# Kernel tuning notes

Hardware: AMD Instinct MI355X
Metric: run time of the kernel (lower is better)

The kernel has to match this reference:

```python
import jax, jax.numpy as jnp
import numpy as np

B, NPG, NFEAT, NHID, NCLASS = 32, 256, 128, 64, 6
N = B * NPG
E_PER = NPG * 16
C = 1.0
SQC = 1.0  # sqrt(c)
MIN_NORM = 1e-15
PROJ_EPS = 4e-3
LAMB = 1.0


def _norm(x):
    return jnp.clip(jnp.linalg.norm(x, axis=-1, keepdims=True), MIN_NORM)


def artanh(x):
    x = jnp.clip(x, -1.0 + 1e-7, 1.0 - 1e-7)
    return 0.5 * (jnp.log1p(x) - jnp.log1p(-x))


def proj(x):
    # clip points to stay inside the Poincare ball
    n = _norm(x)
    maxn = (1.0 - PROJ_EPS) / SQC
    return jnp.where(n > maxn, x / n * maxn, x)


def expmap0(u):
    un = _norm(u)
    return jnp.tanh(SQC * un) * u / (SQC * un)


def logmap0(p):
    pn = _norm(p)
    return artanh(SQC * pn) * p / (SQC * pn)


def mobius_matvec(W, x):
    xn = _norm(x)
    mx = x @ W.T
    mxn = _norm(mx)
    return jnp.tanh(mxn / xn * artanh(SQC * xn)) * mx / (mxn * SQC)


def mobius_add(x, y):
    x2 = jnp.sum(x * x, -1, keepdims=True)
    y2 = jnp.sum(y * y, -1, keepdims=True)
    xy = jnp.sum(x * y, -1, keepdims=True)
    num = (1.0 + 2.0 * C * xy + C * y2) * x + (1.0 - C * x2) * y
    den = 1.0 + 2.0 * C * xy + C * C * x2 * y2
    return num / jnp.clip(den, MIN_NORM)


def hgc_layer(xh, adj, W, b):
    # HypLinear (mobius matvec + hyperbolic bias)
    h = proj(mobius_matvec(W, xh))
    hb = proj(expmap0(b.reshape(1, -1)))
    h = proj(mobius_add(h, hb))
    # HypAgg: aggregate in tangent space at origin
    h = proj(expmap0(adj @ logmap0(h)))
    # HypAct: relu in tangent space
    return proj(expmap0(jax.nn.relu(logmap0(h))))


def hgpsl_pool(x, adj, att, nb, npg):
    deg = adj.sum(-1)
    dis = jnp.where(deg > 0, deg ** -0.5, 0.0)
    prop = dis[:, None] * (adj @ (dis[:, None] * x))
    score = jnp.abs(x - prop).sum(-1)  # [N]
    k = npg // 2
    vals, idx = jax.lax.top_k(score.reshape(nb, npg), k)  # per-graph top-k
    gidx = (idx + (jnp.arange(nb) * npg)[:, None]).reshape(-1)  # global ids
    xn = x[gidx] * jnp.tanh(vals).reshape(-1, 1)
    adj_ind = adj[gidx][:, gidx]
    # structure learning: single-head additive attention, masked per graph
    d = xn.shape[-1]
    e = jax.nn.leaky_relu((xn @ att[:d])[:, None] + (xn @ att[d:])[None, :], 0.2)
    gid = jnp.repeat(jnp.arange(nb), k)
    mask = gid[:, None] == gid[None, :]
    new_adj = jnp.where(mask, jax.nn.relu(e) + LAMB * adj_ind, 0.0)
    return xn, new_adj


def readout(x, nb, k):
    xr = x.reshape(nb, k, -1)
    return jnp.concatenate([xr.max(axis=1), xr.mean(axis=1)], axis=-1)


def to_hyp(t):
    return proj(expmap0(t))  # proj_tan0 is identity on the Poincare ball


def forward(x, edge_index, W1, b1, W2, b2, W3, b3, att1, att2,
            lw1, lb1, lw2, lb2, lw3, lb3):
    row, col = edge_index[0], edge_index[1]
    w = (x[row].sum(-1) + x[col].sum(-1)) * 0.5
    adj1 = jnp.zeros((N, N), x.dtype).at[row, col].set(w)

    t = logmap0(hgc_layer(to_hyp(x), adj1, W1, b1))
    t, adj2 = hgpsl_pool(t, adj1, att1, B, NPG)
    k1 = NPG // 2
    x1 = readout(t, B, k1)

    t = logmap0(hgc_layer(to_hyp(t), adj2, W2, b2))
    t, adj3 = hgpsl_pool(t, adj2, att2, B, k1)
    k2 = k1 // 2
    x2 = readout(t, B, k2)

    t = logmap0(hgc_layer(to_hyp(t), adj3, W3, b3))
    x3 = readout(t, B, k2)

    r = jax.nn.relu(x1) + jax.nn.relu(x2) + jax.nn.relu(x3)
    r = jax.nn.relu(r @ lw1.T + lb1)
    r = jax.nn.relu(r @ lw2.T + lb2)
    return jax.nn.log_softmax(r @ lw3.T + lb3, axis=-1)


def setup_inputs() -> dict:
    key = jax.random.key(0)
    ks = jax.random.split(key, 16)
    s = 0.1
    x = jax.random.normal(ks[0], (N, NFEAT), jnp.float32)
    off = jnp.repeat(jnp.arange(B, dtype=jnp.int32) * NPG, E_PER)
    row = jax.random.randint(ks[1], (B * E_PER,), 0, NPG, jnp.int32) + off
    col = jax.random.randint(ks[2], (B * E_PER,), 0, NPG, jnp.int32) + off
    edge_index = jnp.stack([row, col])
    return {
        "x": x,
        "edge_index": edge_index,
        "W1": jax.random.normal(ks[3], (NHID, NFEAT), jnp.float32) * s,
        "b1": jax.random.normal(ks[4], (NHID,), jnp.float32) * s,
        "W2": jax.random.normal(ks[5], (NHID, NHID), jnp.float32) * s,
        "b2": jax.random.normal(ks[6], (NHID,), jnp.float32) * s,
        "W3": jax.random.normal(ks[7], (NHID, NHID), jnp.float32) * s,
        "b3": jax.random.normal(ks[8], (NHID,), jnp.float32) * s,
        "att1": jax.random.normal(ks[9], (2 * NHID,), jnp.float32) * s,
        "att2": jax.random.normal(ks[10], (2 * NHID,), jnp.float32) * s,
        "lw1": jax.random.normal(ks[11], (NHID, 2 * NHID), jnp.float32) * s,
        "lb1": jnp.zeros((NHID,), jnp.float32),
        "lw2": jax.random.normal(ks[12], (NHID // 2, NHID), jnp.float32) * s,
        "lb2": jnp.zeros((NHID // 2,), jnp.float32),
        "lw3": jax.random.normal(ks[13], (NCLASS, NHID // 2), jnp.float32) * s,
        "lb3": jnp.zeros((NCLASS,), jnp.float32),
    }


def reference(x, edge_index, W1, b1, W2, b2, W3, b3, att1, att2,
              lw1, lb1, lw2, lb2, lw3, lb3):
    return forward(x, edge_index, W1, b1, W2, b2, W3, b3, att1, att2,
                   lw1, lb1, lw2, lb2, lw3, lb3)
```

## Files before the change

kernel.cpp:

```cpp
#include <hip/hip_runtime.h>
#include <math.h>

#define MAXN 0.996f

__device__ __forceinline__ float wredsum(float v) {
#pragma unroll
  for (int o = 32; o > 0; o >>= 1) v += __shfl_xor(v, o);
  return v;
}

__device__ __forceinline__ float artanh_f(float x) {
  x = fminf(fmaxf(x, -1.0f + 1e-7f), 1.0f - 1e-7f);
  return 0.5f * (log1pf(x) - log1pf(-x));
}

__global__ void k_rowsum(const float* __restrict__ x, float* __restrict__ s) {
  const int row = blockIdx.x, j = threadIdx.x;
  float a = x[(size_t)row * 128 + j] + x[(size_t)row * 128 + 64 + j];
  a = wredsum(a);
  if (j == 0) s[row] = a;
}

__global__ void k_edges(const int* __restrict__ er, const int* __restrict__ ec,
                        const float* __restrict__ s, float* __restrict__ adj, int nE) {
  int e = blockIdx.x * blockDim.x + threadIdx.x;
  if (e >= nE) return;
  int r = er[e], c = ec[e];
  int g = r >> 8;
  adj[(((size_t)g * 256) + (r & 255)) * 256 + (c & 255)] = 0.5f * (s[r] + s[c]);
}

template <int IND>
__global__ void k_stageA(const float* __restrict__ x, const float* __restrict__ Wm,
                         const float* __restrict__ b, float* __restrict__ u) {
  const int row = blockIdx.x;
  const int j = threadIdx.x;
  __shared__ float xs[IND];
  for (int t = j; t < IND; t += 64) xs[t] = x[(size_t)row * IND + t];
  __syncthreads();

  float bj = b[j];
  float nb = sqrtf(wredsum(bj * bj));
  float ub = fmaxf(nb, 1e-15f);
  float eb = tanhf(ub) / ub;
  float cb = fmaxf(eb * nb, 1e-15f);
  float hbj = bj * eb * ((cb > MAXN) ? MAXN / cb : 1.0f);
  float y2 = wredsum(hbj * hbj);

  float a2 = 0.f;
  for (int t = j; t < IND; t += 64) a2 += xs[t] * xs[t];
  float nx = sqrtf(wredsum(a2));
  float un = fmaxf(nx, 1e-15f);
  float s1 = tanhf(un) / un;
  float nv = s1 * nx;
  float nn = fmaxf(nv, 1e-15f);
  float s2 = (nn > MAXN) ? MAXN / nn : 1.0f;
  float alpha = s1 * s2;
  float xn = fmaxf(fminf(nn, MAXN), 1e-15f);

  float y = 0.f;
  const float* wr = Wm + (size_t)j * IND;
  for (int t = 0; t < IND; ++t) y += xs[t] * wr[t];
  float mxj = alpha * y;
  float mxn = fmaxf(sqrtf(wredsum(mxj * mxj)), 1e-15f);
  float hj = (tanhf(mxn / xn * artanh_f(xn)) / mxn) * mxj;

  float hn = fmaxf(sqrtf(wredsum(hj * hj)), 1e-15f);
  if (hn > MAXN) hj *= MAXN / hn;

  float x2 = wredsum(hj * hj);
  float xy = wredsum(hj * hbj);
  float num = (1.f + 2.f * xy + y2) * hj + (1.f - x2) * hbj;
  float den = fmaxf(1.f + 2.f * xy + x2 * y2, 1e-15f);
  float aj = num / den;

  float an = fmaxf(sqrtf(wredsum(aj * aj)), 1e-15f);
  float pn = an;
  if (an > MAXN) { aj *= MAXN / an; pn = MAXN; }
  u[(size_t)row * 64 + j] = (artanh_f(pn) / pn) * aj;
}

template <int NPGL>
__global__ void k_stageB(const float* __restrict__ adj, const float* __restrict__ u,
                         float* __restrict__ t, float* __restrict__ dis, int wantDis) {
  const int row = blockIdx.x;
  const int g = row / NPGL;
  const int j = threadIdx.x;
  const float* arow = adj + (size_t)row * NPGL;
  const float* ug = u + (size_t)g * NPGL * 64;
  float acc = 0.f, dsum = 0.f;
  for (int c = 0; c < NPGL; ++c) { float a = arow[c]; acc += a * ug[(size_t)c * 64 + j]; dsum += a; }

  float n0 = sqrtf(wredsum(acc * acc));
  float u0 = fmaxf(n0, 1e-15f);
  float e1 = tanhf(u0) / u0;
  float c1 = fmaxf(e1 * n0, 1e-15f);
  float v = acc * e1;
  if (c1 > MAXN) { v *= MAXN / c1; c1 = MAXN; }
  v *= artanh_f(c1) / c1;
  v = fmaxf(v, 0.f);

  float n2 = sqrtf(wredsum(v * v));
  float u2 = fmaxf(n2, 1e-15f);
  float e2 = tanhf(u2) / u2;
  float c2 = fmaxf(e2 * n2, 1e-15f);
  v *= e2;
  if (c2 > MAXN) { v *= MAXN / c2; c2 = MAXN; }
  v *= artanh_f(c2) / c2;
  t[(size_t)row * 64 + j] = v;
  if (wantDis && j == 0) dis[row] = (dsum > 0.f) ? (1.0f / sqrtf(dsum)) : 0.f;
}

template <int NPGL>
__global__ void k_stageC(const float* __restrict__ adj, const float* __restrict__ t,
                         const float* __restrict__ dis, float* __restrict__ score) {
  const int row = blockIdx.x;
  const int g = row / NPGL;
  const int j = threadIdx.x;
  const float* arow = adj + (size_t)row * NPGL;
  const float* tg = t + (size_t)g * NPGL * 64;
  const float* dg = dis + (size_t)g * NPGL;
  float acc = 0.f;
  for (int c = 0; c < NPGL; ++c) acc += arow[c] * dg[c] * tg[(size_t)c * 64 + j];
  float d = fabsf(t[(size_t)row * 64 + j] - dis[row] * acc);
  d = wredsum(d);
  if (j == 0) score[row] = d;
}

template <int NPGL>
__global__ void k_stageD(const float* __restrict__ score, const float* __restrict__ t,
                         const float* __restrict__ att, float* __restrict__ xn,
                         float* __restrict__ s1o, float* __restrict__ s2o,
                         int* __restrict__ gidx, float* __restrict__ xread) {
  constexpr int K = NPGL / 2;
  const int g = blockIdx.x;
  const int i = threadIdx.x;
  __shared__ float sc[NPGL];
  __shared__ int sel[K];
  __shared__ float sval[K];
  __shared__ float xs[K * 64];
  sc[i] = score[(size_t)g * NPGL + i];
  __syncthreads();
  float si = sc[i];
  int rank = 0;
  for (int c = 0; c < NPGL; ++c) { float v = sc[c]; rank += (v > si) || (v == si && c < i); }
  if (rank < K) { sel[rank] = i; sval[rank] = si; }
  __syncthreads();
  if (i < K) {
    int li = sel[i];
    float tv = tanhf(sval[i]);
    const float* trow = t + ((size_t)g * NPGL + li) * 64;
    float a = 0.f, b = 0.f;
    for (int jj = 0; jj < 64; ++jj) {
      float v = trow[jj] * tv;
      xs[i * 64 + jj] = v;
      a += v * att[jj];
      b += v * att[64 + jj];
    }
    s1o[(size_t)g * K + i] = a;
    s2o[(size_t)g * K + i] = b;
    gidx[(size_t)g * K + i] = li;
    float* xout = xn + ((size_t)g * K + i) * 64;
    for (int jj = 0; jj < 64; ++jj) xout[jj] = xs[i * 64 + jj];
  }
  __syncthreads();
  if (i < 64) {
    float mx = -1e30f, sm = 0.f;
    for (int r = 0; r < K; ++r) { float v = xs[r * 64 + i]; mx = fmaxf(mx, v); sm += v; }
    xread[(size_t)g * 128 + i] = mx;
    xread[(size_t)g * 128 + 64 + i] = sm * (1.0f / K);
  }
}

template <int NPGL>
__global__ void k_stageE(const float* __restrict__ s1, const float* __restrict__ s2,
                         const int* __restrict__ gidx, const float* __restrict__ adj_old,
                         float* __restrict__ adj_new) {
  constexpr int K = NPGL / 2;
  int idx = blockIdx.x * blockDim.x + threadIdx.x;
  if (idx >= 32 * K * K) return;
  int g = idx / (K * K);
  int r = idx - g * K * K;
  int ii = r / K, jj = r - ii * K;
  float e = s1[(size_t)g * K + ii] + s2[(size_t)g * K + jj];
  float v = fmaxf(e, 0.f) +
            adj_old[(((size_t)g * NPGL) + gidx[(size_t)g * K + ii]) * NPGL + gidx[(size_t)g * K + jj]];
  adj_new[(((size_t)g * K) + ii) * K + jj] = v;
}

__global__ void k_readout64(const float* __restrict__ t, float* __restrict__ xread) {
  const int g = blockIdx.x, j = threadIdx.x;
  float mx = -1e30f, sm = 0.f;
  for (int r = 0; r < 64; ++r) { float v = t[((size_t)g * 64 + r) * 64 + j]; mx = fmaxf(mx, v); sm += v; }
  xread[(size_t)g * 128 + j] = mx;
  xread[(size_t)g * 128 + 64 + j] = sm * (1.0f / 64.0f);
}

__global__ void k_mlp(const float* __restrict__ x1, const float* __restrict__ x2,
                      const float* __restrict__ x3, const float* __restrict__ lw1,
                      const float* __restrict__ lb1, const float* __restrict__ lw2,
                      const float* __restrict__ lb2, const float* __restrict__ lw3,
                      const float* __restrict__ lb3, float* __restrict__ out) {
  const int b = blockIdx.x, j = threadIdx.x;
  __shared__ float r[128];
  __shared__ float h1[64];
  __shared__ float h2[32];
  __shared__ float z[6];
  for (int t = j; t < 128; t += 64)
    r[t] = fmaxf(x1[(size_t)b * 128 + t], 0.f) + fmaxf(x2[(size_t)b * 128 + t], 0.f) +
           fmaxf(x3[(size_t)b * 128 + t], 0.f);
  __syncthreads();
  float acc = lb1[j];
  for (int t = 0; t < 128; ++t) acc += r[t] * lw1[(size_t)j * 128 + t];
  h1[j] = fmaxf(acc, 0.f);
  __syncthreads();
  if (j < 32) {
    float a = lb2[j];
    for (int t = 0; t < 64; ++t) a += h1[t] * lw2[(size_t)j * 64 + t];
    h2[j] = fmaxf(a, 0.f);
  }
  __syncthreads();
  if (j < 6) {
    float a = lb3[j];
    for (int t = 0; t < 32; ++t) a += h2[t] * lw3[(size_t)j * 32 + t];
    z[j] = a;
  }
  __syncthreads();
  if (j < 6) {
    float m = z[0];
    for (int c = 1; c < 6; ++c) m = fmaxf(m, z[c]);
    float se = 0.f;
    for (int c = 0; c < 6; ++c) se += expf(z[c] - m);
    out[(size_t)b * 6 + j] = z[j] - m - logf(se);
  }
}

extern "C" void kernel_launch(void* const* d_in, const int* in_sizes, int n_in,
                              void* d_out, int out_size, void* d_ws, size_t ws_size,
                              hipStream_t stream) {
  const float* x = (const float*)d_in[0];
  const int* ei = (const int*)d_in[1];
  const float* W1 = (const float*)d_in[2];
  const float* b1 = (const float*)d_in[3];
  const float* W2 = (const float*)d_in[4];
  const float* b2 = (const float*)d_in[5];
  const float* W3 = (const float*)d_in[6];
  const float* b3 = (const float*)d_in[7];
  const float* att1 = (const float*)d_in[8];
  const float* att2 = (const float*)d_in[9];
  const float* lw1 = (const float*)d_in[10];
  const float* lb1 = (const float*)d_in[11];
  const float* lw2 = (const float*)d_in[12];
  const float* lb2 = (const float*)d_in[13];
  const float* lw3 = (const float*)d_in[14];
  const float* lb3 = (const float*)d_in[15];
  float* out = (float*)d_out;
  const int nE = in_sizes[1] / 2;

  float* p = (float*)d_ws;
  float* srow = p;  p += 8192;
  float* adj1 = p;  p += (size_t)32 * 256 * 256;
  float* adj2 = p;  p += (size_t)32 * 128 * 128;
  float* adj3 = p;  p += (size_t)32 * 64 * 64;
  float* ubuf = p;  p += (size_t)8192 * 64;
  float* t1 = p;    p += (size_t)8192 * 64;
  float* t2 = p;    p += (size_t)4096 * 64;
  float* t3 = p;    p += (size_t)2048 * 64;
  float* dis = p;   p += 8192;
  float* score = p; p += 8192;
  float* xn1 = p;   p += (size_t)4096 * 64;
  float* xn2 = p;   p += (size_t)2048 * 64;
  float* s1b = p;   p += 4096;
  float* s2b = p;   p += 4096;
  float* x1 = p;    p += 32 * 128;
  float* x2 = p;    p += 32 * 128;
  float* x3 = p;    p += 32 * 128;
  int* gidx1 = (int*)p; p += 4096;
  int* gidx2 = (int*)p; p += 2048;

  hipMemsetAsync(adj1, 0, (size_t)32 * 256 * 256 * sizeof(float), stream);
  k_rowsum<<<8192, 64, 0, stream>>>(x, srow);
  k_edges<<<(nE + 255) / 256, 256, 0, stream>>>(ei, ei + nE, srow, adj1, nE);

  k_stageA<128><<<8192, 64, 0, stream>>>(x, W1, b1, ubuf);
  k_stageB<256><<<8192, 64, 0, stream>>>(adj1, ubuf, t1, dis, 1);
  k_stageC<256><<<8192, 64, 0, stream>>>(adj1, t1, dis, score);
  k_stageD<256><<<32, 256, 0, stream>>>(score, t1, att1, xn1, s1b, s2b, gidx1, x1);
  k_stageE<256><<<(32 * 128 * 128 + 255) / 256, 256, 0, stream>>>(s1b, s2b, gidx1, adj1, adj2);

  k_stageA<64><<<4096, 64, 0, stream>>>(xn1, W2, b2, ubuf);
  k_stageB<128><<<4096, 64, 0, stream>>>(adj2, ubuf, t2, dis, 1);
  k_stageC<128><<<4096, 64, 0, stream>>>(adj2, t2, dis, score);
  k_stageD<128><<<32, 128, 0, stream>>>(score, t2, att2, xn2, s1b, s2b, gidx2, x2);
  k_stageE<128><<<(32 * 64 * 64 + 255) / 256, 256, 0, stream>>>(s1b, s2b, gidx2, adj2, adj3);

  k_stageA<64><<<2048, 64, 0, stream>>>(xn2, W3, b3, ubuf);
  k_stageB<64><<<2048, 64, 0, stream>>>(adj3, ubuf, t3, dis, 0);
  k_readout64<<<32, 64, 0, stream>>>(t3, x3);

  k_mlp<<<32, 64, 0, stream>>>(x1, x2, x3, lw1, lb1, lw2, lb2, lw3, lb3, out);
}
```

Measured before the change: 257.4 us.

## Fuse whole pipeline into per-graph megakernel with sparse CSR aggregation

Replaces the chain of about 15 launches with two kernels: a batched first HypLinear stage that also computes row sums, and a per-graph 1024-thread megakernel. The megakernel builds the adjacency, compresses each row into a per-row neighbour list via ballot, runs sparse aggregation and scoring, and does top-k, pooling, the later layers and the MLP head in one block. This removes launch overhead and the dense 256-wide adjacency scans, at the cost of only 32 blocks of parallelism and a 128-entry cap on neighbours per row. It also assumes edges come sorted by graph with an equal count per graph (EPG = nE/32), which the old scatter did not require.

Result: slower. 763.6 us (+196.7%).

```diff
diff --git a/kernel.cpp b/kernel.cpp
--- a/kernel.cpp
+++ b/kernel.cpp
@@ -2,6 +2,18 @@
 #include <math.h>
 
 #define MAXN 0.996f
+#define AR (1 << 18)
+#define O_ADJ1 0
+#define O_ADJ2 65536
+#define O_ADJ3 81920
+#define O_U 86016
+#define O_T 102400
+#define O_DT 118784
+#define O_XN 135168
+#define O_XN2 143360
+#define O_NZW 147456
+#define O_NZC 180224
+#define O_SROW 212992
 
 __device__ __forceinline__ float wredsum(float v) {
 #pragma unroll
@@ -14,83 +26,7 @@
   return 0.5f * (log1pf(x) - log1pf(-x));
 }
 
-__global__ void k_rowsum(const float* __restrict__ x, float* __restrict__ s) {
-  const int row = blockIdx.x, j = threadIdx.x;
-  float a = x[(size_t)row * 128 + j] + x[(size_t)row * 128 + 64 + j];
-  a = wredsum(a);
-  if (j == 0) s[row] = a;
-}
-
-__global__ void k_edges(const int* __restrict__ er, const int* __restrict__ ec,
-                        const float* __restrict__ s, float* __restrict__ adj, int nE) {
-  int e = blockIdx.x * blockDim.x + threadIdx.x;
-  if (e >= nE) return;
-  int r = er[e], c = ec[e];
-  int g = r >> 8;
-  adj[(((size_t)g * 256) + (r & 255)) * 256 + (c & 255)] = 0.5f * (s[r] + s[c]);
-}
-
-template <int IND>
-__global__ void k_stageA(const float* __restrict__ x, const float* __restrict__ Wm,
-                         const float* __restrict__ b, float* __restrict__ u) {
-  const int row = blockIdx.x;
-  const int j = threadIdx.x;
-  __shared__ float xs[IND];
-  for (int t = j; t < IND; t += 64) xs[t] = x[(size_t)row * IND + t];
-  __syncthreads();
-
-  float bj = b[j];
-  float nb = sqrtf(wredsum(bj * bj));
-  float ub = fmaxf(nb, 1e-15f);
-  float eb = tanhf(ub) / ub;
-  float cb = fmaxf(eb * nb, 1e-15f);
-  float hbj = bj * eb * ((cb > MAXN) ? MAXN / cb : 1.0f);
-  float y2 = wredsum(hbj * hbj);
-
-  float a2 = 0.f;
-  for (int t = j; t < IND; t += 64) a2 += xs[t] * xs[t];
-  float nx = sqrtf(wredsum(a2));
-  float un = fmaxf(nx, 1e-15f);
-  float s1 = tanhf(un) / un;
-  float nv = s1 * nx;
-  float nn = fmaxf(nv, 1e-15f);
-  float s2 = (nn > MAXN) ? MAXN / nn : 1.0f;
-  float alpha = s1 * s2;
-  float xn = fmaxf(fminf(nn, MAXN), 1e-15f);
-
-  float y = 0.f;
-  const float* wr = Wm + (size_t)j * IND;
-  for (int t = 0; t < IND; ++t) y += xs[t] * wr[t];
-  float mxj = alpha * y;
-  float mxn = fmaxf(sqrtf(wredsum(mxj * mxj)), 1e-15f);
-  float hj = (tanhf(mxn / xn * artanh_f(xn)) / mxn) * mxj;
-
-  float hn = fmaxf(sqrtf(wredsum(hj * hj)), 1e-15f);
-  if (hn > MAXN) hj *= MAXN / hn;
-
-  float x2 = wredsum(hj * hj);
-  float xy = wredsum(hj * hbj);
-  float num = (1.f + 2.f * xy + y2) * hj + (1.f - x2) * hbj;
-  float den = fmaxf(1.f + 2.f * xy + x2 * y2, 1e-15f);
-  float aj = num / den;
-
-  float an = fmaxf(sqrtf(wredsum(aj * aj)), 1e-15f);
-  float pn = an;
-  if (an > MAXN) { aj *= MAXN / an; pn = MAXN; }
-  u[(size_t)row * 64 + j] = (artanh_f(pn) / pn) * aj;
-}
-
-template <int NPGL>
-__global__ void k_stageB(const float* __restrict__ adj, const float* __restrict__ u,
-                         float* __restrict__ t, float* __restrict__ dis, int wantDis) {
-  const int row = blockIdx.x;
-  const int g = row / NPGL;
-  const int j = threadIdx.x;
-  const float* arow = adj + (size_t)row * NPGL;
-  const float* ug = u + (size_t)g * NPGL * 64;
-  float acc = 0.f, dsum = 0.f;
-  for (int c = 0; c < NPGL; ++c) { float a = arow[c]; acc += a * ug[(size_t)c * 64 + j]; dsum += a; }
-
+__device__ __forceinline__ float bchain(float acc) {
   float n0 = sqrtf(wredsum(acc * acc));
   float u0 = fmaxf(n0, 1e-15f);
   float e1 = tanhf(u0) / u0;
@@ -99,7 +35,6 @@
   if (c1 > MAXN) { v *= MAXN / c1; c1 = MAXN; }
   v *= artanh_f(c1) / c1;
   v = fmaxf(v, 0.f);
-
   float n2 = sqrtf(wredsum(v * v));
   float u2 = fmaxf(n2, 1e-15f);
   float e2 = tanhf(u2) / u2;
@@ -107,131 +42,341 @@
   v *= e2;
   if (c2 > MAXN) { v *= MAXN / c2; c2 = MAXN; }
   v *= artanh_f(c2) / c2;
-  t[(size_t)row * 64 + j] = v;
-  if (wantDis && j == 0) dis[row] = (dsum > 0.f) ? (1.0f / sqrtf(dsum)) : 0.f;
+  return v;
+}
+
+__global__ __launch_bounds__(256) void k_A1srow(const float* __restrict__ x,
+                                                const float* __restrict__ W1,
+                                                const float* __restrict__ b1,
+                                                float* __restrict__ ws) {
+  constexpr int IND = 128, WSTR = 132;
+  __shared__ float Wl[64 * WSTR];
+  __shared__ float xsh[8 * IND];
+  const int tid = threadIdx.x, w = tid >> 6, j = tid & 63;
+  const int rowBase = blockIdx.x * 8;
+  const int g = rowBase >> 8;
+  float* Aa = ws + (size_t)g * AR;
+  for (int f = tid; f < 64 * IND; f += 256) { int jj = f >> 7, t = f & 127; Wl[jj * WSTR + t] = W1[f]; }
+  for (int f = tid; f < 8 * IND; f += 256) xsh[f] = x[(size_t)rowBase * IND + f];
+  __syncthreads();
+  float bj = b1[j];
+  float nb = sqrtf(wredsum(bj * bj));
+  float ub = fmaxf(nb, 1e-15f), eb = tanhf(ub) / ub, cb = fmaxf(eb * nb, 1e-15f);
+  float hbj = bj * eb * ((cb > MAXN) ? MAXN / cb : 1.0f);
+  float y2 = wredsum(hbj * hbj);
+  const float4* wrow = (const float4*)(Wl + j * WSTR);
+#pragma unroll
+  for (int rr = 0; rr < 2; ++rr) {
+    const int lr = w * 2 + rr;
+    const float* xs = xsh + lr * IND;
+    float v0 = xs[j], v1 = xs[64 + j];
+    float sr = wredsum(v0 + v1);
+    float a2 = wredsum(v0 * v0 + v1 * v1);
+    float nx = sqrtf(a2);
+    float un = fmaxf(nx, 1e-15f);
+    float s1 = tanhf(un) / un;
+    float nv = s1 * nx;
+    float nn = fmaxf(nv, 1e-15f);
+    float s2 = (nn > MAXN) ? MAXN / nn : 1.0f;
+    float alpha = s1 * s2;
+    float xnm = fmaxf(fminf(nn, MAXN), 1e-15f);
+    const float4* xv4 = (const float4*)xs;
+    float y = 0.f;
+#pragma unroll
+    for (int t4 = 0; t4 < IND / 4; ++t4) {
+      float4 w4 = wrow[t4];
+      float4 v4 = xv4[t4];
+      y += w4.x * v4.x + w4.y * v4.y + w4.z * v4.z + w4.w * v4.w;
+    }
+    float mxj = alpha * y;
+    float mxn = fmaxf(sqrtf(wredsum(mxj * mxj)), 1e-15f);
+    float hj = (tanhf(mxn / xnm * artanh_f(xnm)) / mxn) * mxj;
+    float hn = fmaxf(sqrtf(wredsum(hj * hj)), 1e-15f);
+    if (hn > MAXN) hj *= MAXN / hn;
+    float x2v = wredsum(hj * hj);
+    float xyv = wredsum(hj * hbj);
+    float num = (1.f + 2.f * xyv + y2) * hj + (1.f - x2v) * hbj;
+    float den = fmaxf(1.f + 2.f * xyv + x2v * y2, 1e-15f);
+    float aj = num / den;
+    float an = fmaxf(sqrtf(wredsum(aj * aj)), 1e-15f);
+    float pn = an;
+    if (an > MAXN) { aj *= MAXN / an; pn = MAXN; }
+    const int lrow = (rowBase & 255) + lr;
+    if (j == 0) Aa[O_SROW + lrow] = sr;
+    Aa[O_U + (size_t)lrow * 64 + j] = (artanh_f(pn) / pn) * aj;
+  }
+}
+
+template <int R>
+__device__ void csr_build(const float* adjm, int* nzc, float* nzw, int* cntS, float* disS,
+                          int w, int j) {
+  constexpr int RPW = R / 16;
+  unsigned long long below = (j == 0) ? 0ull : ((1ull << j) - 1ull);
+#pragma unroll
+  for (int i = 0; i < RPW; ++i) {
+    int r = w * RPW + i;
+    int base = 0;
+    float ds = 0.f;
+    for (int ch = 0; ch < R / 64; ++ch) {
+      int c = ch * 64 + j;
+      float v = adjm[(size_t)r * R + c];
+      ds += v;
+      unsigned long long m = __ballot(v != 0.f);
+      int pos = base + __popcll(m & below);
+      if (v != 0.f && pos < 128) { nzc[r * 128 + pos] = c; nzw[r * 128 + pos] = v; }
+      base += __popcll(m);
+    }
+    ds = wredsum(ds);
+    if (j == 0) {
+      cntS[r] = base < 128 ? base : 128;
+      disS[r] = (ds > 0.f) ? (1.0f / sqrtf(ds)) : 0.f;
+    }
+  }
+}
+
+template <int ROWS>
+__device__ void stageB_sparse(const int* nzc, const float* nzw, const int* cntS,
+                              const float* disS, const float* uin, float* tout, float* dtout,
+                              int wantDis, int w, int j) {
+  constexpr int RPW = ROWS / 16;
+#pragma unroll
+  for (int i = 0; i < RPW; ++i) {
+    int r = w * RPW + i;
+    int cnt = cntS[r];
+    const int* rc = nzc + r * 128;
+    const float* rw = nzw + r * 128;
+    float acc = 0.f;
+    for (int k = 0; k < cnt; ++k) acc += rw[k] * uin[(size_t)rc[k] * 64 + j];
+    float v = bchain(acc);
+    tout[(size_t)r * 64 + j] = v;
+    if (wantDis) dtout[(size_t)r * 64 + j] = disS[r] * v;
+  }
+}
+
+template <int ROWS>
+__device__ void stageC_sparse(const int* nzc, const float* nzw, const int* cntS,
+                              const float* disS, const float* tin, const float* dtin,
+                              float* scS, int w, int j) {
+  constexpr int RPW = ROWS / 16;
+#pragma unroll
+  for (int i = 0; i < RPW; ++i) {
+    int r = w * RPW + i;
+    int cnt = cntS[r];
+    const int* rc = nzc + r * 128;
+    const float* rw = nzw + r * 128;
+    float acc = 0.f;
+    for (int k = 0; k < cnt; ++k) acc += rw[k] * dtin[(size_t)rc[k] * 64 + j];
+    float d = fabsf(tin[(size_t)r * 64 + j] - disS[r] * acc);
+    d = wredsum(d);
+    if (j == 0) scS[r] = d;
+  }
 }
 
 template <int NPGL>
-__global__ void k_stageC(const float* __restrict__ adj, const float* __restrict__ t,
-                         const float* __restrict__ dis, float* __restrict__ score) {
-  const int row = blockIdx.x;
-  const int g = row / NPGL;
-  const int j = threadIdx.x;
-  const float* arow = adj + (size_t)row * NPGL;
-  const float* tg = t + (size_t)g * NPGL * 64;
-  const float* dg = dis + (size_t)g * NPGL;
-  float acc = 0.f;
-  for (int c = 0; c < NPGL; ++c) acc += arow[c] * dg[c] * tg[(size_t)c * 64 + j];
-  float d = fabsf(t[(size_t)row * 64 + j] - dis[row] * acc);
-  d = wredsum(d);
-  if (j == 0) score[row] = d;
+__device__ void stageD(const float* scS, const float* tin, const float* attp, float* xout,
+                       float* s1S, float* s2S, int* selS, float* svalS, int tid, int w, int j) {
+  constexpr int K = NPGL / 2;
+  if (tid < NPGL) {
+    float si = scS[tid];
+    int rank = 0;
+    for (int c = 0; c < NPGL; ++c) { float vv = scS[c]; rank += (vv > si) || (vv == si && c < tid); }
+    if (rank < K) { selS[rank] = tid; svalS[rank] = si; }
+  }
+  __syncthreads();
+  constexpr int RPW = K / 16;
+  float a1 = attp[j], a2v = attp[64 + j];
+#pragma unroll
+  for (int i = w * RPW; i < w * RPW + RPW; ++i) {
+    int li = selS[i];
+    float tv = tanhf(svalS[i]);
+    float v = tin[(size_t)li * 64 + j] * tv;
+    xout[(size_t)i * 64 + j] = v;
+    float sa = wredsum(v * a1);
+    float sb = wredsum(v * a2v);
+    if (j == 0) { s1S[i] = sa; s2S[i] = sb; }
+  }
+  __syncthreads();
 }
 
 template <int NPGL>
-__global__ void k_stageD(const float* __restrict__ score, const float* __restrict__ t,
-                         const float* __restrict__ att, float* __restrict__ xn,
-                         float* __restrict__ s1o, float* __restrict__ s2o,
-                         int* __restrict__ gidx, float* __restrict__ xread) {
+__device__ void stageE(const float* s1S, const float* s2S, const int* selS,
+                       const float* adjO, float* adjN, int tid) {
   constexpr int K = NPGL / 2;
-  const int g = blockIdx.x;
-  const int i = threadIdx.x;
-  __shared__ float sc[NPGL];
-  __shared__ int sel[K];
-  __shared__ float sval[K];
-  __shared__ float xs[K * 64];
-  sc[i] = score[(size_t)g * NPGL + i];
-  __syncthreads();
-  float si = sc[i];
-  int rank = 0;
-  for (int c = 0; c < NPGL; ++c) { float v = sc[c]; rank += (v > si) || (v == si && c < i); }
-  if (rank < K) { sel[rank] = i; sval[rank] = si; }
-  __syncthreads();
-  if (i < K) {
-    int li = sel[i];
-    float tv = tanhf(sval[i]);
-    const float* trow = t + ((size_t)g * NPGL + li) * 64;
-    float a = 0.f, b = 0.f;
-    for (int jj = 0; jj < 64; ++jj) {
-      float v = trow[jj] * tv;
-      xs[i * 64 + jj] = v;
-      a += v * att[jj];
-      b += v * att[64 + jj];
+  for (int idx = tid; idx < K * K; idx += 1024) {
+    int ii = idx / K, jj = idx - ii * K;
+    float e = s1S[ii] + s2S[jj];
+    adjN[idx] = fmaxf(e, 0.f) + adjO[(size_t)selS[ii] * NPGL + selS[jj]];
+  }
+}
+
+template <int K>
+__device__ void readoutK(const float* xrows, float* xS, int tid) {
+  if (tid < 64) {
+    float mx = -1e30f, sm = 0.f;
+    for (int r = 0; r < K; ++r) { float v = xrows[(size_t)r * 64 + tid]; mx = fmaxf(mx, v); sm += v; }
+    xS[tid] = mx;
+    xS[64 + tid] = sm * (1.0f / K);
+  }
+}
+
+template <int ROWS>
+__device__ void stageA64(const float* xin, const float* Wp, const float* bp, float* SM,
+                         float* uout, int tid, int w, int j) {
+  __syncthreads();
+  for (int idx = tid; idx < 64 * 64; idx += 1024) { int jj = idx >> 6, t = idx & 63; SM[t * 65 + jj] = Wp[idx]; }
+  __syncthreads();
+  float bj = bp[j];
+  float nb = sqrtf(wredsum(bj * bj));
+  float ub = fmaxf(nb, 1e-15f), eb = tanhf(ub) / ub, cb = fmaxf(eb * nb, 1e-15f);
+  float hbj = bj * eb * ((cb > MAXN) ? MAXN / cb : 1.0f);
+  float y2 = wredsum(hbj * hbj);
+  constexpr int RPW = ROWS / 16;
+  float xr[RPW], acc[RPW];
+#pragma unroll
+  for (int i = 0; i < RPW; ++i) { xr[i] = xin[(size_t)(w * RPW + i) * 64 + j]; acc[i] = 0.f; }
+#pragma unroll 8
+  for (int t = 0; t < 64; ++t) {
+    float wv = SM[t * 65 + j];
+#pragma unroll
+    for (int i = 0; i < RPW; ++i) acc[i] += __shfl(xr[i], t) * wv;
+  }
+#pragma unroll
+  for (int i = 0; i < RPW; ++i) {
+    int r = w * RPW + i;
+    float a2 = wredsum(xr[i] * xr[i]);
+    float nx = sqrtf(a2);
+    float un = fmaxf(nx, 1e-15f);
+    float s1 = tanhf(un) / un;
+    float nv = s1 * nx;
+    float nn = fmaxf(nv, 1e-15f);
+    float s2 = (nn > MAXN) ? MAXN / nn : 1.0f;
+    float alpha = s1 * s2;
+    float xnm = fmaxf(fminf(nn, MAXN), 1e-15f);
+    float mxj = alpha * acc[i];
+    float mxn = fmaxf(sqrtf(wredsum(mxj * mxj)), 1e-15f);
+    float hj = (tanhf(mxn / xnm * artanh_f(xnm)) / mxn) * mxj;
+    float hn = fmaxf(sqrtf(wredsum(hj * hj)), 1e-15f);
+    if (hn > MAXN) hj *= MAXN / hn;
+    float x2v = wredsum(hj * hj);
+    float xyv = wredsum(hj * hbj);
+    float num = (1.f + 2.f * xyv + y2) * hj + (1.f - x2v) * hbj;
+    float den = fmaxf(1.f + 2.f * xyv + x2v * y2, 1e-15f);
+    float aj = num / den;
+    float an = fmaxf(sqrtf(wredsum(aj * aj)), 1e-15f);
+    float pn = an;
+    if (an > MAXN) { aj *= MAXN / an; pn = MAXN; }
+    uout[(size_t)r * 64 + j] = (artanh_f(pn) / pn) * aj;
+  }
+  __syncthreads();
+}
+
+__global__ __launch_bounds__(1024) void k_mega(
+    const int* __restrict__ er, const int* __restrict__ ec, int EPG,
+    const float* __restrict__ W2, const float* __restrict__ b2,
+    const float* __restrict__ W3, const float* __restrict__ b3,
+    const float* __restrict__ att1, const float* __restrict__ att2,
+    const float* __restrict__ lw1, const float* __restrict__ lb1,
+    const float* __restrict__ lw2, const float* __restrict__ lb2,
+    const float* __restrict__ lw3, const float* __restrict__ lb3,
+    float* __restrict__ ws, float* __restrict__ out) {
+  const int g = blockIdx.x, tid = threadIdx.x, w = tid >> 6, j = tid & 63;
+  float* Aa = ws + (size_t)g * AR;
+  float* adj1 = Aa + O_ADJ1;
+  float* adj2 = Aa + O_ADJ2;
+  float* adj3 = Aa + O_ADJ3;
+  float* u = Aa + O_U;
+  float* tb = Aa + O_T;
+  float* dt = Aa + O_DT;
+  float* xn = Aa + O_XN;
+  float* xn2 = Aa + O_XN2;
+  float* nzw = Aa + O_NZW;
+  int* nzc = (int*)(Aa + O_NZC);
+  float* srow = Aa + O_SROW;
+
+  __shared__ float SM[64 * 65];
+  __shared__ float scS[256];
+  __shared__ float disS[256];
+  __shared__ int cntS[256];
+  __shared__ float svalS[128];
+  __shared__ int selS[128];
+  __shared__ float s1S[128], s2S[128];
+  __shared__ float x1S[128], x2S[128], x3S[128];
+  __shared__ float rS[128], h1S[64], h2S[32], zS[8];
+
+  {
+    float4 z = {0.f, 0.f, 0.f, 0.f};
+    float4* a4 = (float4*)adj1;
+    for (int i = tid; i < 16384; i += 1024) a4[i] = z;
+  }
+  __syncthreads();
+  for (int e = tid; e < EPG; e += 1024) {
+    int ge = g * EPG + e;
+    int r = er[ge] & 255, c = ec[ge] & 255;
+    adj1[r * 256 + c] = 0.5f * (srow[r] + srow[c]);
+  }
+  __syncthreads();
+  csr_build<256>(adj1, nzc, nzw, cntS, disS, w, j);
+  __syncthreads();
+  stageB_sparse<256>(nzc, nzw, cntS, disS, u, tb, dt, 1, w, j);
+  __syncthreads();
+  stageC_sparse<256>(nzc, nzw, cntS, disS, tb, dt, scS, w, j);
+  __syncthreads();
+  stageD<256>(scS, tb, att1, xn, s1S, s2S, selS, svalS, tid, w, j);
+  stageE<256>(s1S, s2S, selS, adj1, adj2, tid);
+  readoutK<128>(xn, x1S, tid);
+  __syncthreads();
+  stageA64<128>(xn, W2, b2, SM, u, tid, w, j);
+  csr_build<128>(adj2, nzc, nzw, cntS, disS, w, j);
+  __syncthreads();
+  stageB_sparse<128>(nzc, nzw, cntS, disS, u, tb, dt, 1, w, j);
+  __syncthreads();
+  stageC_sparse<128>(nzc, nzw, cntS, disS, tb, dt, scS, w, j);
+  __syncthreads();
+  stageD<128>(scS, tb, att2, xn2, s1S, s2S, selS, svalS, tid, w, j);
+  stageE<128>(s1S, s2S, selS, adj2, adj3, tid);
+  readoutK<64>(xn2, x2S, tid);
+  __syncthreads();
+  stageA64<64>(xn2, W3, b3, SM, u, tid, w, j);
+  {
+#pragma unroll
+    for (int i = 0; i < 4; ++i) {
+      int r = w * 4 + i;
+      float arow = adj3[(size_t)r * 64 + j];
+      float acc = 0.f;
+#pragma unroll 16
+      for (int c = 0; c < 64; ++c) acc += __shfl(arow, c) * u[(size_t)c * 64 + j];
+      tb[(size_t)r * 64 + j] = bchain(acc);
     }
-    s1o[(size_t)g * K + i] = a;
-    s2o[(size_t)g * K + i] = b;
-    gidx[(size_t)g * K + i] = li;
-    float* xout = xn + ((size_t)g * K + i) * 64;
-    for (int jj = 0; jj < 64; ++jj) xout[jj] = xs[i * 64 + jj];
-  }
-  __syncthreads();
-  if (i < 64) {
-    float mx = -1e30f, sm = 0.f;
-    for (int r = 0; r < K; ++r) { float v = xs[r * 64 + i]; mx = fmaxf(mx, v); sm += v; }
-    xread[(size_t)g * 128 + i] = mx;
-    xread[(size_t)g * 128 + 64 + i] = sm * (1.0f / K);
-  }
-}
-
-template <int NPGL>
-__global__ void k_stageE(const float* __restrict__ s1, const float* __restrict__ s2,
-                         const int* __restrict__ gidx, const float* __restrict__ adj_old,
-                         float* __restrict__ adj_new) {
-  constexpr int K = NPGL / 2;
-  int idx = blockIdx.x * blockDim.x + threadIdx.x;
-  if (idx >= 32 * K * K) return;
-  int g = idx / (K * K);
-  int r = idx - g * K * K;
-  int ii = r / K, jj = r - ii * K;
-  float e = s1[(size_t)g * K + ii] + s2[(size_t)g * K + jj];
-  float v = fmaxf(e, 0.f) +
-            adj_old[(((size_t)g * NPGL) + gidx[(size_t)g * K + ii]) * NPGL + gidx[(size_t)g * K + jj]];
-  adj_new[(((size_t)g * K) + ii) * K + jj] = v;
-}
-
-__global__ void k_readout64(const float* __restrict__ t, float* __restrict__ xread) {
-  const int g = blockIdx.x, j = threadIdx.x;
-  float mx = -1e30f, sm = 0.f;
-  for (int r = 0; r < 64; ++r) { float v = t[((size_t)g * 64 + r) * 64 + j]; mx = fmaxf(mx, v); sm += v; }
-  xread[(size_t)g * 128 + j] = mx;
-  xread[(size_t)g * 128 + 64 + j] = sm * (1.0f / 64.0f);
-}
-
-__global__ void k_mlp(const float* __restrict__ x1, const float* __restrict__ x2,
-                      const float* __restrict__ x3, const float* __restrict__ lw1,
-                      const float* __restrict__ lb1, const float* __restrict__ lw2,
-                      const float* __restrict__ lb2, const float* __restrict__ lw3,
-                      const float* __restrict__ lb3, float* __restrict__ out) {
-  const int b = blockIdx.x, j = threadIdx.x;
-  __shared__ float r[128];
-  __shared__ float h1[64];
-  __shared__ float h2[32];
-  __shared__ float z[6];
-  for (int t = j; t < 128; t += 64)
-    r[t] = fmaxf(x1[(size_t)b * 128 + t], 0.f) + fmaxf(x2[(size_t)b * 128 + t], 0.f) +
-           fmaxf(x3[(size_t)b * 128 + t], 0.f);
-  __syncthreads();
-  float acc = lb1[j];
-  for (int t = 0; t < 128; ++t) acc += r[t] * lw1[(size_t)j * 128 + t];
-  h1[j] = fmaxf(acc, 0.f);
-  __syncthreads();
-  if (j < 32) {
-    float a = lb2[j];
-    for (int t = 0; t < 64; ++t) a += h1[t] * lw2[(size_t)j * 64 + t];
-    h2[j] = fmaxf(a, 0.f);
-  }
-  __syncthreads();
-  if (j < 6) {
-    float a = lb3[j];
-    for (int t = 0; t < 32; ++t) a += h2[t] * lw3[(size_t)j * 32 + t];
-    z[j] = a;
-  }
-  __syncthreads();
-  if (j < 6) {
-    float m = z[0];
-    for (int c = 1; c < 6; ++c) m = fmaxf(m, z[c]);
+  }
+  __syncthreads();
+  readoutK<64>(tb, x3S, tid);
+  __syncthreads();
+  if (tid < 128) rS[tid] = fmaxf(x1S[tid], 0.f) + fmaxf(x2S[tid], 0.f) + fmaxf(x3S[tid], 0.f);
+  __syncthreads();
+  if (tid < 64) {
+    float a = lb1[tid];
+    for (int t = 0; t < 128; ++t) a += rS[t] * lw1[(size_t)tid * 128 + t];
+    h1S[tid] = fmaxf(a, 0.f);
+  }
+  __syncthreads();
+  if (tid < 32) {
+    float a = lb2[tid];
+    for (int t = 0; t < 64; ++t) a += h1S[t] * lw2[(size_t)tid * 64 + t];
+    h2S[tid] = fmaxf(a, 0.f);
+  }
+  __syncthreads();
+  if (tid < 6) {
+    float a = lb3[tid];
+    for (int t = 0; t < 32; ++t) a += h2S[t] * lw3[(size_t)tid * 32 + t];
+    zS[tid] = a;
+  }
+  __syncthreads();
+  if (tid < 6) {
+    float m = zS[0];
+    for (int c = 1; c < 6; ++c) m = fmaxf(m, zS[c]);
     float se = 0.f;
-    for (int c = 0; c < 6; ++c) se += expf(z[c] - m);
-    out[(size_t)b * 6 + j] = z[j] - m - logf(se);
+    for (int c = 0; c < 6; ++c) se += expf(zS[c] - m);
+    out[(size_t)g * 6 + tid] = zS[tid] - m - logf(se);
   }
 }
 
@@ -255,48 +400,11 @@
   const float* lw3 = (const float*)d_in[14];
   const float* lb3 = (const float*)d_in[15];
   float* out = (float*)d_out;
+  float* ws = (float*)d_ws;
   const int nE = in_sizes[1] / 2;
-
-  float* p = (float*)d_ws;
-  float* srow = p;  p += 8192;
-  float* adj1 = p;  p += (size_t)32 * 256 * 256;
-  float* adj2 = p;  p += (size_t)32 * 128 * 128;
-  float* adj3 = p;  p += (size_t)32 * 64 * 64;
-  float* ubuf = p;  p += (size_t)8192 * 64;
-  float* t1 = p;    p += (size_t)8192 * 64;
-  float* t2 = p;    p += (size_t)4096 * 64;
-  float* t3 = p;    p += (size_t)2048 * 64;
-  float* dis = p;   p += 8192;
-  float* score = p; p += 8192;
-  float* xn1 = p;   p += (size_t)4096 * 64;
-  float* xn2 = p;   p += (size_t)2048 * 64;
-  float* s1b = p;   p += 4096;
-  float* s2b = p;   p += 4096;
-  float* x1 = p;    p += 32 * 128;
-  float* x2 = p;    p += 32 * 128;
-  float* x3 = p;    p += 32 * 128;
-  int* gidx1 = (int*)p; p += 4096;
-  int* gidx2 = (int*)p; p += 2048;
-
-  hipMemsetAsync(adj1, 0, (size_t)32 * 256 * 256 * sizeof(float), stream);
-  k_rowsum<<<8192, 64, 0, stream>>>(x, srow);
-  k_edges<<<(nE + 255) / 256, 256, 0, stream>>>(ei, ei + nE, srow, adj1, nE);
-
-  k_stageA<128><<<8192, 64, 0, stream>>>(x, W1, b1, ubuf);
-  k_stageB<256><<<8192, 64, 0, stream>>>(adj1, ubuf, t1, dis, 1);
-  k_stageC<256><<<8192, 64, 0, stream>>>(adj1, t1, dis, score);
-  k_stageD<256><<<32, 256, 0, stream>>>(score, t1, att1, xn1, s1b, s2b, gidx1, x1);
-  k_stageE<256><<<(32 * 128 * 128 + 255) / 256, 256, 0, stream>>>(s1b, s2b, gidx1, adj1, adj2);
-
-  k_stageA<64><<<4096, 64, 0, stream>>>(xn1, W2, b2, ubuf);
-  k_stageB<128><<<4096, 64, 0, stream>>>(adj2, ubuf, t2, dis, 1);
-  k_stageC<128><<<4096, 64, 0, stream>>>(adj2, t2, dis, score);
-  k_stageD<128><<<32, 128, 0, stream>>>(score, t2, att2, xn2, s1b, s2b, gidx2, x2);
-  k_stageE<128><<<(32 * 64 * 64 + 255) / 256, 256, 0, stream>>>(s1b, s2b, gidx2, adj2, adj3);
-
-  k_stageA<64><<<2048, 64, 0, stream>>>(xn2, W3, b3, ubuf);
-  k_stageB<64><<<2048, 64, 0, stream>>>(adj3, ubuf, t3, dis, 0);
-  k_readout64<<<32, 64, 0, stream>>>(t3, x3);
-
-  k_mlp<<<32, 64, 0, stream>>>(x1, x2, x3, lw1, lb1, lw2, lb2, lw3, lb3, out);
-}
+  const int EPG = nE / 32;
+
+  k_A1srow<<<1024, 256, 0, stream>>>(x, W1, b1, ws);
+  k_mega<<<32, 1024, 0, stream>>>(ei, ei + nE, EPG, W2, b2, W3, b3, att1, att2,
+                                  lw1, lb1, lw2, lb2, lw3, lb3, ws, out);
+}
```
